# Kernel optimization log

Hardware: AMD Instinct MI355X
Metric: run time of the kernel (lower is better)

The kernel has to match this reference:

```python
import jax, jax.numpy as jnp
import numpy as np

N_BINS = 15  # matches __init__ default


def setup_inputs() -> dict:
    key = jax.random.key(0)
    k1, k2 = jax.random.split(key)
    N, C = 100000, 1000
    softmaxes_probs = jax.random.uniform(k1, (N, C), dtype=jnp.float32)
    labels = jax.random.randint(k2, (N,), 0, C, dtype=jnp.int64)
    return {"softmaxes_probs": softmaxes_probs, "labels": labels}


def reference(softmaxes_probs, labels):
    # Classwise ECE: for each class c and bin b = (b/n_bins, (b+1)/n_bins],
    #   sce_c = sum_b |avg_conf_in_bin - acc_in_bin| * (count_in_bin / N)
    # returned value is mean_c sce_c.
    n_bins = N_BINS
    N, C = softmaxes_probs.shape
    conf = softmaxes_probs  # [N, C]

    # bin index: conf in (b/n_bins, (b+1)/n_bins] -> b ; conf <= 0 -> -1 (no bin)
    bin_idx = jnp.ceil(conf * n_bins).astype(jnp.int32) - 1
    bin_idx = jnp.minimum(bin_idx, n_bins - 1)
    valid = bin_idx >= 0

    class_ids = jnp.arange(C, dtype=jnp.int32)[None, :]  # [1, C]
    # combined segment id per (sample, class); invalid entries go to a dump segment
    seg = jnp.where(valid, bin_idx + class_ids * n_bins, C * n_bins)  # [N, C]
    seg_flat = seg.ravel()
    num_seg = C * n_bins + 1

    ones = jnp.ones_like(conf)
    counts = jax.ops.segment_sum(ones.ravel(), seg_flat, num_segments=num_seg)[:-1].reshape(C, n_bins)
    conf_sum = jax.ops.segment_sum(conf.ravel(), seg_flat, num_segments=num_seg)[:-1].reshape(C, n_bins)
    # labels_in_class broadcast to [N, C]
    correct = (labels[:, None] == jnp.arange(C, dtype=labels.dtype)[None, :]).astype(conf.dtype)
    correct_sum = jax.ops.segment_sum(correct.ravel(), seg_flat, num_segments=num_seg)[:-1].reshape(C, n_bins)

    prop_in_bin = counts / N  # prop_in_bin = in_bin.float().mean() over N samples
    nonempty = counts > 0
    denom = jnp.maximum(counts, 1.0)
    acc_in_bin = correct_sum / denom
    avg_conf_in_bin = conf_sum / denom
    contrib = jnp.where(nonempty, jnp.abs(avg_conf_in_bin - acc_in_bin) * prop_in_bin, 0.0)
    per_class_sce = jnp.sum(contrib, axis=1)  # [C]
    return jnp.mean(per_class_sce)
```

## Files before the change

kernel.cpp:

```cpp
#include <hip/hip_runtime.h>


#define NBINS   15
#define THREADS 512
#define PSTRIDE 31
#define LDSW    (THREADS * PSTRIDE)
#define SLABH   (THREADS * NBINS)
#define RBLK    120
#define Q40     1099511627776.0f

typedef float f2_t __attribute__((ext_vector_type(2)));

__global__ __launch_bounds__(THREADS, 4) void ece_hist(
    const float* __restrict__ probs, const int* __restrict__ labels,
    int N, int C, int R,
    unsigned* __restrict__ partial,
    unsigned long long* __restrict__ accum,
    unsigned* __restrict__ doneCnt)
{
    __shared__ unsigned sA[LDSW];
    const int t = threadIdx.x;
    if (blockIdx.x == 0 && t == 0) { *accum = 0ull; *doneCnt = 0u; }
    #pragma unroll
    for (int i = t; i < LDSW; i += THREADS) sA[i] = 0u;
    __syncthreads();

    const int cls0 = 2 * t;
    const bool live = (cls0 + 1 < C);
    const int col  = live ? cls0 : 0;

    const int r0 = blockIdx.x * R;
    int rend = N - r0; if (rend > R) rend = R; if (rend < 0) rend = 0;

    const f2_t* p = (const f2_t*)(probs + (size_t)r0 * C + col);
    const size_t rowstep = (size_t)(C >> 1);
    unsigned* s0 = sA + t * PSTRIDE;

    const f2_t zf = {0.0f, 0.0f};
    f2_t bufA[8], bufB[8];
    int  labA[8], labB[8];

    #define LOADG(buf, lab, base)                                           \
        _Pragma("unroll")                                                   \
        for (int k = 0; k < 8; ++k) {                                       \
            buf[k] = live ? __builtin_nontemporal_load(                     \
                                &p[(size_t)((base) + k) * rowstep]) : zf;   \
            lab[k] = labels[r0 + (base) + k];        \
        }

    #define PROC1(v, lb)                                                    \
        {                                                                   \
            int b0 = (int)(v.x * 15.0f);    \
            b0 = b0 < NBINS - 1 ? b0 : NBINS - 1;                           \
            unsigned c0 = (unsigned)fmaf(v.x, 128.0f, 0.5f);                \
            c0 += ((lb) == cls0) ? (unsigned)(-128) : 0u;                   \
            atomicAdd(&s0[b0], (v.x > 0.0f) ? c0 : 0u);                     \
            int b1 = (int)(v.y * 15.0f);                                    \
            b1 = b1 < NBINS - 1 ? b1 : NBINS - 1;                           \
            unsigned c1 = (unsigned)fmaf(v.y, 128.0f, 0.5f);                \
            c1 += ((lb) == cls0 + 1) ? (unsigned)(-128) : 0u;               \
            atomicAdd(&s0[NBINS + b1], (v.y > 0.0f) ? c1 : 0u);             \
        }

    #define PROCG(buf, lab)                                                 \
        _Pragma("unroll")                                                   \
        for (int k = 0; k < 8; ++k) PROC1(buf[k], lab[k])

    int r = 0;
    if (rend >= 24) {
        LOADG(bufA, labA, 0);
        const int nFull = (rend - 8) >> 4;
        for (int g = 0; g < nFull; ++g) {
            LOADG(bufB, labB, 16 * g + 8);
            PROCG(bufA, labA);
            LOADG(bufA, labA, 16 * g + 16);
            PROCG(bufB, labB);
        }
        PROCG(bufA, labA);
        r = 16 * nFull + 8;
    } else if (rend >= 8) {
        LOADG(bufA, labA, 0);
        PROCG(bufA, labA);
        r = 8;
    }
    for (; r < rend; ++r) {
        f2_t v = live ? p[(size_t)r * rowstep] : zf;
        int lb = labels[r0 + r];
        PROC1(v, lb);
    }
    __syncthreads();

    unsigned* dst = partial + (size_t)blockIdx.x * SLABH;
    #pragma unroll
    for (int i = t; i < SLABH; i += THREADS) {
        int owner = i / 15, j = 2 * (i - owner * 15);
        unsigned v0 = sA[owner * PSTRIDE + j];
        unsigned v1 = sA[owner * PSTRIDE + j + 1];
        dst[i] = (v0 & 0xFFFFu) | (v1 << 16);
    }
}

__global__ __launch_bounds__(1024, 1) void ece_red(
    const unsigned* __restrict__ partial, int chunks, int C, int N,
    unsigned long long* __restrict__ accum, unsigned* __restrict__ doneCnt,
    float* __restrict__ out)
{
    __shared__ int sq0[16][64];
    __shared__ int sq1[16][64];
    const int t = threadIdx.x;
    const int g = t >> 6, pj = t & 63;
    const int pair = blockIdx.x * 64 + pj;

    const int gsz = (chunks + 15) >> 4;
    int k0 = g * gsz;
    int k1 = k0 + gsz; if (k1 > chunks) k1 = chunks;
    int a0 = 0, a1 = 0;
    #pragma unroll 8
    for (int k = k0; k < k1; ++k) {
        unsigned w = partial[(size_t)k * SLABH + pair];
        a0 += (int)(short)(w & 0xFFFFu);
        a1 += (int)(short)(w >> 16);
    }
    sq0[g][pj] = a0;
    sq1[g][pj] = a1;
    __syncthreads();

    if (t < 64) {
        int t0 = 0, t1 = 0;
        #pragma unroll
        for (int gg = 0; gg < 16; ++gg) { t0 += sq0[gg][t]; t1 += sq1[gg][t]; }
        int slot0 = (blockIdx.x * 64 + t) * 2;
        float contrib = 0.0f;
        if (slot0     < C * NBINS) contrib += fabsf((float)t0);
        if (slot0 + 1 < C * NBINS) contrib += fabsf((float)t1);
        contrib *= (1.0f / 128.0f) * (1.0f / (float)N);
        for (int o = 32; o; o >>= 1) contrib += __shfl_down(contrib, o);
        if (t == 0) {
            atomicAdd(accum, (unsigned long long)(contrib * Q40));
            __threadfence();
            if (atomicAdd(doneCnt, 1u) == (unsigned)(RBLK - 1)) {
                __threadfence();
                unsigned long long a = atomicAdd(accum, 0ull);
                out[0] = (float)((double)a * (1.0 / (double)Q40) / (double)C);
            }
        }
    }
}

extern "C" void kernel_launch(void* const* d_in, const int* in_sizes, int n_in,
                              void* d_out, int out_size, void* d_ws, size_t ws_size,
                              hipStream_t stream) {
    const float* probs  = (const float*)d_in[0];
    const int*   labels = (const int*)d_in[1];
    const int N = in_sizes[1];
    const int C = in_sizes[0] / N;

    const size_t headBytes = 4096;
    const size_t slabBytes = (size_t)SLABH * 4;

    unsigned long long* accum   = (unsigned long long*)d_ws;
    unsigned*           doneCnt = (unsigned*)((char*)d_ws + 8);
    unsigned*           partial = (unsigned*)((char*)d_ws + headBytes);

    long long avail = (long long)ws_size - (long long)headBytes;
    int chunks = (int)(avail / (long long)slabBytes);
    if (chunks > 500) chunks = 500;
    if (chunks < 393) chunks = 393;
    const int R = (N + chunks - 1) / chunks;

    ece_hist<<<chunks, THREADS, 0, stream>>>(probs, labels, N, C, R,
                                             partial, accum, doneCnt);
    ece_red<<<RBLK, 1024, 0, stream>>>(partial, chunks, C, N,
                                       accum, doneCnt, (float*)d_out);
}
```

Baseline: 86.50 us.

## Fuse histogram and reduction kernels using last-blocks ticket scheme

Merges the separate reduction kernel into the histogram kernel. Each block takes a ticket after writing its partial slab, and the last RBLK blocks spin until all blocks finish and then perform the cross-chunk reduction with 512 threads, using 8 waves instead of 16 groups. The counters are now zeroed by a memset before launch instead of inside the kernel. This removes one kernel launch and the gap between the two kernels, but adds spin-waiting, a memset call, and halves the reduction parallelism per block.

```diff
diff --git a/kernel.cpp b/kernel.cpp
--- a/kernel.cpp
+++ b/kernel.cpp
@@ -11,16 +11,18 @@
 
 typedef float f2_t __attribute__((ext_vector_type(2)));
 
-__global__ __launch_bounds__(THREADS, 4) void ece_hist(
+__global__ __launch_bounds__(THREADS, 4) void ece_fused(
     const float* __restrict__ probs, const int* __restrict__ labels,
-    int N, int C, int R,
+    int N, int C, int R, int chunks,
     unsigned* __restrict__ partial,
     unsigned long long* __restrict__ accum,
-    unsigned* __restrict__ doneCnt)
+    unsigned* __restrict__ doneCnt,
+    unsigned* __restrict__ doneRed,
+    float* __restrict__ out)
 {
     __shared__ unsigned sA[LDSW];
+    __shared__ unsigned sTicket;
     const int t = threadIdx.x;
-    if (blockIdx.x == 0 && t == 0) { *accum = 0ull; *doneCnt = 0u; }
     #pragma unroll
     for (int i = t; i < LDSW; i += THREADS) sA[i] = 0u;
     __syncthreads();
@@ -98,21 +100,27 @@
         unsigned v1 = sA[owner * PSTRIDE + j + 1];
         dst[i] = (v0 & 0xFFFFu) | (v1 << 16);
     }
-}
 
-__global__ __launch_bounds__(1024, 1) void ece_red(
-    const unsigned* __restrict__ partial, int chunks, int C, int N,
-    unsigned long long* __restrict__ accum, unsigned* __restrict__ doneCnt,
-    float* __restrict__ out)
-{
-    __shared__ int sq0[16][64];
-    __shared__ int sq1[16][64];
-    const int t = threadIdx.x;
-    const int g = t >> 6, pj = t & 63;
-    const int pair = blockIdx.x * 64 + pj;
+    __threadfence();
+    if (t == 0) sTicket = atomicAdd(doneCnt, 1u);
+    __syncthreads();
+    const int ticket = (int)sTicket;
+    if (ticket < chunks - RBLK) return;
 
-    const int gsz = (chunks + 15) >> 4;
-    int k0 = g * gsz;
+    const int rb = ticket - (chunks - RBLK);
+    if (t == 0) {
+        while (atomicAdd(doneCnt, 0u) < (unsigned)chunks)
+            __builtin_amdgcn_s_sleep(8);
+    }
+    __syncthreads();
+    __threadfence();
+
+    int* sq0 = (int*)sA;
+    int* sq1 = (int*)(sA + 512);
+    const int wave = t >> 6, lane = t & 63;
+    const int pair = rb * 64 + lane;
+    const int gsz = (chunks + 7) >> 3;
+    int k0 = wave * gsz;
     int k1 = k0 + gsz; if (k1 > chunks) k1 = chunks;
     int a0 = 0, a1 = 0;
     #pragma unroll 8
@@ -121,15 +129,15 @@
         a0 += (int)(short)(w & 0xFFFFu);
         a1 += (int)(short)(w >> 16);
     }
-    sq0[g][pj] = a0;
-    sq1[g][pj] = a1;
+    sq0[wave * 64 + lane] = a0;
+    sq1[wave * 64 + lane] = a1;
     __syncthreads();
 
     if (t < 64) {
         int t0 = 0, t1 = 0;
         #pragma unroll
-        for (int gg = 0; gg < 16; ++gg) { t0 += sq0[gg][t]; t1 += sq1[gg][t]; }
-        int slot0 = (blockIdx.x * 64 + t) * 2;
+        for (int g = 0; g < 8; ++g) { t0 += sq0[g * 64 + t]; t1 += sq1[g * 64 + t]; }
+        int slot0 = (rb * 64 + t) * 2;
         float contrib = 0.0f;
         if (slot0     < C * NBINS) contrib += fabsf((float)t0);
         if (slot0 + 1 < C * NBINS) contrib += fabsf((float)t1);
@@ -138,7 +146,7 @@
         if (t == 0) {
             atomicAdd(accum, (unsigned long long)(contrib * Q40));
             __threadfence();
-            if (atomicAdd(doneCnt, 1u) == (unsigned)(RBLK - 1)) {
+            if (atomicAdd(doneRed, 1u) == (unsigned)(RBLK - 1)) {
                 __threadfence();
                 unsigned long long a = atomicAdd(accum, 0ull);
                 out[0] = (float)((double)a * (1.0 / (double)Q40) / (double)C);
@@ -160,6 +168,7 @@
 
     unsigned long long* accum   = (unsigned long long*)d_ws;
     unsigned*           doneCnt = (unsigned*)((char*)d_ws + 8);
+    unsigned*           doneRed = (unsigned*)((char*)d_ws + 12);
     unsigned*           partial = (unsigned*)((char*)d_ws + headBytes);
 
     long long avail = (long long)ws_size - (long long)headBytes;
@@ -168,8 +177,8 @@
     if (chunks < 393) chunks = 393;
     const int R = (N + chunks - 1) / chunks;
 
-    ece_hist<<<chunks, THREADS, 0, stream>>>(probs, labels, N, C, R,
-                                             partial, accum, doneCnt);
-    ece_red<<<RBLK, 1024, 0, stream>>>(partial, chunks, C, N,
-                                       accum, doneCnt, (float*)d_out);
+    hipMemsetAsync(d_ws, 0, 64, stream);
+    ece_fused<<<chunks, THREADS, 0, stream>>>(probs, labels, N, C, R, chunks,
+                                              partial, accum, doneCnt, doneRed,
+                                              (float*)d_out);
 }
```

Result: slower. 249.4 us (+188.3%).
